# Performance work log

Hardware: AMD Instinct MI355X
Metric: run time of the kernel (lower is better)

## Reference

```python
import jax, jax.numpy as jnp
import numpy as np

# Nemotron-H Mamba2 mixer decoder layer (prefill path, zero initial states,
# full context lengths). Dims per init_kwargs.
B, S, H = 1, 256, 4096
NH, P, G, N, K = 128, 64, 8, 128, 4   # num_heads, head_dim, n_groups, ssm_state_size, conv_kernel
D_INNER = NH * P                      # 8192
D_STATE = G * N                       # 1024
CONV_DIM = D_INNER + 2 * D_STATE      # 10240
IN_OUT = D_INNER + CONV_DIM + NH      # 18560
EPS = 1e-6


def setup_inputs() -> dict:
    key = jax.random.key(0)
    ks = jax.random.split(key, 8)
    sc = 0.02
    return {
        "hidden_states": jax.random.normal(ks[0], (B, S, H), jnp.float32),
        "conv_state": jnp.zeros((B, CONV_DIM, K - 1), jnp.float32),
        "ssm_state": jnp.zeros((B, NH, P, N), jnp.float32),
        "norm_weight": jnp.ones((H,), jnp.float32),
        "w_in": jax.random.normal(ks[1], (IN_OUT, H), jnp.float32) * sc,
        "conv_w": jax.random.normal(ks[2], (CONV_DIM, K), jnp.float32) * 0.2,
        "conv_b": jnp.zeros((CONV_DIM,), jnp.float32),
        "A_log": jax.random.uniform(ks[3], (NH,), jnp.float32, 0.0, 1.0),
        "D_param": jax.random.normal(ks[4], (NH,), jnp.float32) * 0.1,
        "dt_bias": jax.random.normal(ks[5], (NH,), jnp.float32) * 0.1,
        "ssm_norm_weight": jnp.ones((D_INNER,), jnp.float32),
        "w_out": jax.random.normal(ks[6], (H, D_INNER), jnp.float32) * sc,
    }


def _rmsnorm(x, w, eps=EPS):
    var = jnp.mean(x * x, axis=-1, keepdims=True)
    return x * jax.lax.rsqrt(var + eps) * w


def reference(hidden_states, conv_state, ssm_state, norm_weight, w_in, conv_w,
              conv_b, A_log, D_param, dt_bias, ssm_norm_weight, w_out):
    resid = hidden_states
    h = _rmsnorm(hidden_states, norm_weight)           # pre-mixer RMSNorm
    proj = jnp.einsum('bsh,oh->bso', h, w_in)          # in_proj [B,S,18560]
    gate = proj[..., :D_INNER]
    xconv = proj[..., D_INNER:D_INNER + CONV_DIM]
    dt = proj[..., D_INNER + CONV_DIM:]                # [B,S,NH]

    # depthwise causal conv1d, initial left context = conv_state
    xc = jnp.swapaxes(xconv, 1, 2)                     # [B,CONV_DIM,S]
    xpad = jnp.concatenate([conv_state, xc], axis=-1)  # [B,CONV_DIM,S+K-1]
    conv_state_out = xpad[:, :, -(K - 1):]
    y = conv_b[None, :, None]
    for j in range(K):                                 # K=4 taps, unrolled
        y = y + conv_w[:, j][None, :, None] * xpad[:, :, j:j + S]
    y = jax.nn.silu(jnp.swapaxes(y, 1, 2))             # [B,S,CONV_DIM]

    xs = y[..., :D_INNER].reshape(B, S, NH, P)
    Bs = y[..., D_INNER:D_INNER + D_STATE].reshape(B, S, G, N)
    Cs = y[..., D_INNER + D_STATE:].reshape(B, S, G, N)

    A = -jnp.exp(A_log)                                # [NH]
    dtp = jax.nn.softplus(dt + dt_bias)                # [B,S,NH]
    rep = NH // G
    Bh = jnp.repeat(Bs, rep, axis=2)                   # [B,S,NH,N]
    Ch = jnp.repeat(Cs, rep, axis=2)

    def step(state, inp):
        x_t, b_t, c_t, dt_t = inp                      # [B,NH,P],[B,NH,N],[B,NH,N],[B,NH]
        dA = jnp.exp(dt_t * A)                         # [B,NH]
        state = state * dA[..., None, None] + (dt_t[..., None] * x_t)[..., None] * b_t[:, :, None, :]
        y_t = jnp.einsum('bhpn,bhn->bhp', state, c_t)
        return state, y_t

    inps = (jnp.swapaxes(xs, 0, 1), jnp.swapaxes(Bh, 0, 1),
            jnp.swapaxes(Ch, 0, 1), jnp.swapaxes(dtp, 0, 1))
    ssm_state_out, ys = jax.lax.scan(step, ssm_state, inps)
    ys = jnp.swapaxes(ys, 0, 1) + D_param[None, None, :, None] * xs
    ssm_out = ys.reshape(B, S, D_INNER)

    # gated grouped RMSNorm (group_size = D_INNER // G = 1024)
    gated = ssm_out * jax.nn.silu(gate)
    gsize = D_INNER // G
    gg = gated.reshape(B, S, D_INNER // gsize, gsize)
    var = jnp.mean(gg * gg, axis=-1, keepdims=True)
    normed = (gg * jax.lax.rsqrt(var + EPS)).reshape(B, S, D_INNER) * ssm_norm_weight

    out = jnp.einsum('bsd,hd->bsh', normed, w_out)     # out_proj
    return resid + out, conv_state_out, ssm_state_out
```

## Files before the change

### kernel.cpp

```cpp
#include <hip/hip_runtime.h>
#include <hip/hip_bf16.h>

#define Sq 256
#define Hd 4096
#define NH 128
#define Pd 64
#define Gg 8
#define Nn 128
#define D_INNER 8192
#define D_STATE 1024
#define CONV_DIM 10240
#define IN_OUT 18560
#define DT_COL0 18432
#define EPSI 1e-6f

typedef _Float16 f16x8 __attribute__((ext_vector_type(8)));
typedef _Float16 f16x2 __attribute__((ext_vector_type(2)));
typedef float f32x4 __attribute__((ext_vector_type(4)));

__device__ inline ushort f2h(float f) {
  _Float16 h = (_Float16)f;
  return __builtin_bit_cast(ushort, h);
}
__device__ inline float h2f(ushort u) {
  return (float)__builtin_bit_cast(_Float16, u);
}
__device__ inline ushort f2h_lo(float f, ushort hi) {
  float hf = (float)__builtin_bit_cast(_Float16, hi);
  _Float16 l = (_Float16)(f - hf);
  return __builtin_bit_cast(ushort, l);
}
__device__ inline f16x2 pkrtz(float a, float b) {
  return __builtin_bit_cast(f16x2, __builtin_amdgcn_cvt_pkrtz(a, b));
}

__global__ __launch_bounds__(256) void rmsnorm_k(const float* __restrict__ x,
                                                 const float* __restrict__ w,
                                                 ushort* __restrict__ h_hi,
                                                 ushort* __restrict__ h_lo) {
  int s = blockIdx.x, t = threadIdx.x;
  const float4* row = reinterpret_cast<const float4*>(x + (size_t)s * Hd);
  const float4* wv  = reinterpret_cast<const float4*>(w);
  float4 v[4];
  float ss = 0.f;
#pragma unroll
  for (int i = 0; i < 4; i++) {
    v[i] = row[t + i * 256];
    ss += v[i].x * v[i].x + v[i].y * v[i].y + v[i].z * v[i].z + v[i].w * v[i].w;
  }
#pragma unroll
  for (int off = 32; off > 0; off >>= 1) ss += __shfl_xor(ss, off);
  __shared__ float red[4];
  if ((t & 63) == 0) red[t >> 6] = ss;
  __syncthreads();
  ss = red[0] + red[1] + red[2] + red[3];
  float scale = rsqrtf(ss * (1.f / (float)Hd) + EPSI);
  ushort4* hh = reinterpret_cast<ushort4*>(h_hi + (size_t)s * Hd);
  ushort4* hl = reinterpret_cast<ushort4*>(h_lo + (size_t)s * Hd);
#pragma unroll
  for (int i = 0; i < 4; i++) {
    float4 wi = wv[t + i * 256];
    float f0 = v[i].x * scale * wi.x, f1 = v[i].y * scale * wi.y;
    float f2 = v[i].z * scale * wi.z, f3 = v[i].w * scale * wi.w;
    ushort4 oh, ol;
    oh.x = f2h(f0); ol.x = f2h_lo(f0, oh.x);
    oh.y = f2h(f1); ol.y = f2h_lo(f1, oh.y);
    oh.z = f2h(f2); ol.z = f2h_lo(f2, oh.z);
    oh.w = f2h(f3); ol.w = f2h_lo(f3, oh.w);
    hh[t + i * 256] = oh;
    hl[t + i * 256] = ol;
  }
}

__global__ __launch_bounds__(512) void gemm_w256(const ushort* __restrict__ A,
                                                 const float* __restrict__ B,
                                                 float* __restrict__ C0,
                                                 ushort* __restrict__ Cp,
                                                 int ldc, int K, int kLen) {
  __shared__ __align__(16) ushort As[2][256 * 32];
  __shared__ __align__(16) ushort Bs[2][128 * 32];
  int t = threadIdx.x;
  int wave = t >> 6, lane = t & 63;
  int wr = wave >> 1, wc = wave & 1;
  int frow = lane & 15, gq = lane >> 4;
  int bcol = blockIdx.x * 128;
  int z = blockIdx.z;
  int kStart = z * kLen;

  int ar = t >> 2;
  int ax = (ar >> 1) & 3;
  const ushort* ApG0 = A + (size_t)ar * K + kStart + ((t & 3) ^ ax) * 8;
  const ushort* ApG1 = ApG0 + (size_t)128 * K;
  char* dstA0 = (char*)&As[0][0] + wave * 1024;
  char* dstA1 = (char*)&As[0][0] + 8192 + wave * 1024;

  int brow = t >> 2, bq4 = t & 3;
  int bx = (brow >> 1) & 3;
  const float* BpG = B + (size_t)(bcol + brow) * K + kStart + bq4 * 8;
  int bslot = ((bq4) ^ bx) * 16;
  float4 rb[2];

  f32x4 acc[4][4] = {};
  const int NT = kLen / 32;

#define ISSUE_B(kk) { rb[0] = *(const float4*)(BpG + (kk)); \
                      rb[1] = *(const float4*)(BpG + (kk) + 4); }
#define DMA_A(p, kk) { \
    __builtin_amdgcn_global_load_lds( \
        (const __attribute__((address_space(1))) void*)(ApG0 + (kk)), \
        (__attribute__((address_space(3))) void*)(dstA0 + (p) * 16384), 16, 0, 0); \
    __builtin_amdgcn_global_load_lds( \
        (const __attribute__((address_space(1))) void*)(ApG1 + (kk)), \
        (__attribute__((address_space(3))) void*)(dstA1 + (p) * 16384), 16, 0, 0); }
#define WRITE_B(p) { \
    union { f16x2 h2[4]; uint4 q; } u; \
    u.h2[0] = pkrtz(rb[0].x, rb[0].y); u.h2[1] = pkrtz(rb[0].z, rb[0].w); \
    u.h2[2] = pkrtz(rb[1].x, rb[1].y); u.h2[3] = pkrtz(rb[1].z, rb[1].w); \
    *(uint4*)((char*)&Bs[0][0] + (p) * 8192 + brow * 64 + bslot) = u.q; }

  ISSUE_B(0)
  DMA_A(0, 0)
  WRITE_B(0)
  __syncthreads();

  for (int i = 0; i < NT; ++i) {
    int cur = i & 1;
    if (i + 1 < NT) {
      ISSUE_B((i + 1) * 32)
      DMA_A(cur ^ 1, (i + 1) * 32)
    }
    f16x8 af[4], bf[4];
#pragma unroll
    for (int m = 0; m < 4; ++m) {
      int row = wr * 64 + m * 16 + frow;
      af[m] = *(const f16x8*)((const char*)&As[0][0] + cur * 16384 + row * 64 +
                              ((gq ^ ((row >> 1) & 3)) * 16));
    }
#pragma unroll
    for (int n = 0; n < 4; ++n) {
      int row = wc * 64 + n * 16 + frow;
      bf[n] = *(const f16x8*)((const char*)&Bs[0][0] + cur * 8192 + row * 64 +
                              ((gq ^ ((row >> 1) & 3)) * 16));
    }
#pragma unroll
    for (int m = 0; m < 4; ++m)
#pragma unroll
      for (int n = 0; n < 4; ++n)
        acc[m][n] = __builtin_amdgcn_mfma_f32_16x16x32_f16(af[m], bf[n], acc[m][n], 0, 0, 0);
    __builtin_amdgcn_sched_barrier(0);
    if (i + 1 < NT) WRITE_B(cur ^ 1)
    __syncthreads();
  }
#undef ISSUE_B
#undef DMA_A
#undef WRITE_B

  if (z == 0) {
#pragma unroll
    for (int m = 0; m < 4; ++m) {
      int row0 = wr * 64 + m * 16 + (lane >> 4) * 4;
#pragma unroll
      for (int n = 0; n < 4; ++n) {
        int col = bcol + wc * 64 + n * 16 + frow;
#pragma unroll
        for (int r = 0; r < 4; ++r)
          C0[(size_t)(row0 + r) * ldc + col] = acc[m][n][r];
      }
    }
  } else {
    ushort* Cz = Cp + (size_t)(z - 1) * Sq * ldc;
#pragma unroll
    for (int m = 0; m < 4; ++m) {
      int row0 = wr * 64 + m * 16 + (lane >> 4) * 4;
#pragma unroll
      for (int n = 0; n < 4; ++n) {
        int col = bcol + wc * 64 + n * 16 + frow;
#pragma unroll
        for (int r = 0; r < 4; ++r)
          Cz[(size_t)(row0 + r) * ldc + col] = f2h(acc[m][n][r]);
      }
    }
  }
}

template<int BN, bool SPLIT>
__global__ __launch_bounds__(256) void gemm_mfma(const ushort* __restrict__ A_hi,
                                                 const ushort* __restrict__ A_lo,
                                                 const float* __restrict__ B,
                                                 float* __restrict__ C,
                                                 int ldc, int K, int kLen,
                                                 int bcol0, int M) {
  constexpr int BK = 64;
  constexpr int LDA = 72;
  constexpr int N_REP = BN / 32;
  constexpr int BQN = (BN == 128) ? 8 : 4;
  __shared__ __align__(16) ushort As[64 * LDA];
  __shared__ __align__(16) ushort Bs[BN * LDA];
  __shared__ __align__(16) ushort AsL[SPLIT ? 64 * LDA : 1];
  __shared__ __align__(16) ushort BsL[SPLIT ? BN * LDA : 1];

  int t = threadIdx.x;
  int wave = t >> 6, lane = t & 63;
  int wr = wave >> 1, wc = wave & 1;
  int frow = lane & 15, fk = (lane >> 4) * 8;
  int rowBase = blockIdx.x * 64;
  int bcol = bcol0 + blockIdx.y * BN;
  int ccol = blockIdx.y * BN;
  int kStart = blockIdx.z * kLen;
  C += (size_t)blockIdx.z * M * ldc;

  int arow = t >> 2, ak = (t & 3) * 16;
  const ushort* Ap  = A_hi + (size_t)(rowBase + arow) * K + ak;
  const ushort* ApL = SPLIT ? (A_lo + (size_t)(rowBase + arow) * K + ak) : nullptr;

  int brow, bq;
  if constexpr (BN == 128) { brow = t >> 1; bq = (t & 1) * 32; }
  else                     { brow = t >> 2; bq = (t & 3) * 16; }
  const float* Bp = B + (size_t)(bcol + brow) * K + bq;

  f32x4 acc[2][N_REP] = {};
  uint4 aPre[2], aPreL[2];
  float4 bPre[BQN];

  auto loadK = [&](int kk) {
    aPre[0] = *reinterpret_cast<const uint4*>(Ap + kk);
    aPre[1] = *reinterpret_cast<const uint4*>(Ap + kk + 8);
    if constexpr (SPLIT) {
      aPreL[0] = *reinterpret_cast<const uint4*>(ApL + kk);
      aPreL[1] = *reinterpret_cast<const uint4*>(ApL + kk + 8);
    }
#pragma unroll
    for (int j = 0; j < BQN; ++j)
      bPre[j] = *reinterpret_cast<const float4*>(Bp + kk + j * 4);
  };

  loadK(kStart);
  for (int ki = 0; ki < kLen; ki += BK) {
    __syncthreads();
    *reinterpret_cast<uint4*>(&As[arow * LDA + ak])     = aPre[0];
    *reinterpret_cast<uint4*>(&As[arow * LDA + ak + 8]) = aPre[1];
    if constexpr (SPLIT) {
      *reinterpret_cast<uint4*>(&AsL[arow * LDA + ak])     = aPreL[0];
      *reinterpret_cast<uint4*>(&AsL[arow * LDA + ak + 8]) = aPreL[1];
    }
    {
      ushort hb[BQN * 4];
      ushort lb[SPLIT ? BQN * 4 : 1];
      const float* bf = reinterpret_cast<const float*>(bPre);
#pragma unroll
      for (int j = 0; j < BQN * 4; ++j) {
        hb[j] = f2h(bf[j]);
        if constexpr (SPLIT) lb[j] = f2h_lo(bf[j], hb[j]);
      }
#pragma unroll
      for (int j = 0; j < BQN / 2; ++j)
        *reinterpret_cast<uint4*>(&Bs[brow * LDA + bq + j * 8]) =
            reinterpret_cast<const uint4*>(hb)[j];
      if constexpr (SPLIT) {
#pragma unroll
        for (int j = 0; j < BQN / 2; ++j)
          *reinterpret_cast<uint4*>(&BsL[brow * LDA + bq + j * 8]) =
              reinterpret_cast<const uint4*>(lb)[j];
      }
    }
    __syncthreads();
    if (ki + BK < kLen) loadK(kStart + ki + BK);
    f16x8 af[2][2], bfv[N_REP][2];
    f16x8 afL[SPLIT ? 2 : 1][2], bfL[SPLIT ? N_REP : 1][2];
#pragma unroll
    for (int m = 0; m < 2; ++m)
#pragma unroll
      for (int kh = 0; kh < 2; ++kh) {
        af[m][kh] = *reinterpret_cast<const f16x8*>(
            &As[(wr * 32 + m * 16 + frow) * LDA + kh * 32 + fk]);
        if constexpr (SPLIT)
          afL[m][kh] = *reinterpret_cast<const f16x8*>(
              &AsL[(wr * 32 + m * 16 + frow) * LDA + kh * 32 + fk]);
      }
#pragma unroll
    for (int n = 0; n < N_REP; ++n)
#pragma unroll
      for (int kh = 0; kh < 2; ++kh) {
        bfv[n][kh] = *reinterpret_cast<const f16x8*>(
            &Bs[(wc * (BN / 2) + n * 16 + frow) * LDA + kh * 32 + fk]);
        if constexpr (SPLIT)
          bfL[n][kh] = *reinterpret_cast<const f16x8*>(
              &BsL[(wc * (BN / 2) + n * 16 + frow) * LDA + kh * 32 + fk]);
      }
#pragma unroll
    for (int kh = 0; kh < 2; ++kh)
#pragma unroll
      for (int m = 0; m < 2; ++m)
#pragma unroll
        for (int n = 0; n < N_REP; ++n) {
          acc[m][n] = __builtin_amdgcn_mfma_f32_16x16x32_f16(af[m][kh], bfv[n][kh], acc[m][n], 0, 0, 0);
          if constexpr (SPLIT) {
            acc[m][n] = __builtin_amdgcn_mfma_f32_16x16x32_f16(af[m][kh], bfL[n][kh], acc[m][n], 0, 0, 0);
            acc[m][n] = __builtin_amdgcn_mfma_f32_16x16x32_f16(afL[m][kh], bfv[n][kh], acc[m][n], 0, 0, 0);
          }
        }
  }

#pragma unroll
  for (int m = 0; m < 2; ++m) {
    int row0 = rowBase + wr * 32 + m * 16 + (lane >> 4) * 4;
#pragma unroll
    for (int n = 0; n < N_REP; ++n) {
      int col = ccol + wc * (BN / 2) + n * 16 + frow;
#pragma unroll
      for (int r = 0; r < 4; ++r)
        C[(size_t)(row0 + r) * ldc + col] = acc[m][n][r];
    }
  }
}

__global__ __launch_bounds__(256) void reduce_in_k(float* __restrict__ proj,
                                                   const ushort* __restrict__ pp) {
  int i = blockIdx.x * 256 + threadIdx.x;
  const size_t PL = (size_t)Sq * IN_OUT;
  float4 o = reinterpret_cast<const float4*>(proj)[i];
#pragma unroll
  for (int zz = 0; zz < 3; ++zz) {
    ushort4 hv = reinterpret_cast<const ushort4*>(pp + zz * PL)[i];
    o.x += h2f(hv.x); o.y += h2f(hv.y); o.z += h2f(hv.z); o.w += h2f(hv.w);
  }
  reinterpret_cast<float4*>(proj)[i] = o;
}

__global__ __launch_bounds__(256) void conv_silu_k(const float* __restrict__ proj,
                                                   const float* __restrict__ cstate,
                                                   const float* __restrict__ cw,
                                                   const float* __restrict__ cb,
                                                   float* __restrict__ y,
                                                   float* __restrict__ out1) {
  int s = blockIdx.y;
  if (s == Sq) {
    int c = blockIdx.x * 256 + threadIdx.x;
#pragma unroll
    for (int tt = 0; tt < 3; ++tt)
      out1[c * 3 + tt] = proj[(size_t)(Sq - 3 + tt) * IN_OUT + D_INNER + c];
    return;
  }
  int c = blockIdx.x * 256 + threadIdx.x;
  float acc = cb[c];
  float4 w4 = *reinterpret_cast<const float4*>(cw + c * 4);
  float wj[4] = {w4.x, w4.y, w4.z, w4.w};
#pragma unroll
  for (int j = 0; j < 4; j++) {
    int si = s + j - 3;
    float v = (si < 0) ? cstate[c * 3 + (si + 3)]
                       : proj[(size_t)si * IN_OUT + D_INNER + c];
    acc += wj[j] * v;
  }
  float sig = 1.f / (1.f + expf(-acc));
  y[(size_t)s * CONV_DIM + c] = acc * sig;
}

#define CS 16
__global__ __launch_bounds__(256) void ssm_scan_k(const float* __restrict__ y_conv,
                                                  const float* __restrict__ dtfix,
                                                  const float* __restrict__ dt_bias,
                                                  const float* __restrict__ sstate_in,
                                                  const float* __restrict__ A_log,
                                                  const float* __restrict__ D_param,
                                                  float* __restrict__ ys_out,
                                                  float* __restrict__ sstate_out) {
  int h = blockIdx.x >> 2;
  int pb = (blockIdx.x & 3) * 16;
  int t = threadIdx.x;
  int ng = t & 15, pl = t >> 4;
  int g = h >> 4;
  float A = -expf(A_log[h]);
  float Dp = D_param[h];
  float bias = dt_bias[h];

  float st[8];
  {
    const float* sp = sstate_in + ((size_t)h * Pd + pb + pl) * Nn + ng * 8;
    float4 v = *reinterpret_cast<const float4*>(sp);
    float4 w = *reinterpret_cast<const float4*>(sp + 4);
    st[0] = v.x; st[1] = v.y; st[2] = v.z; st[3] = v.w;
    st[4] = w.x; st[5] = w.y; st[6] = w.z; st[7] = w.w;
  }

  __shared__ __align__(16) float ybuf[CS][272];
  __shared__ float dts[CS];
  int lr = t >> 4;
  int lc = t & 15;

  for (int ch = 0; ch < Sq / CS; ++ch) {
    int s0 = ch * CS;
    __syncthreads();
    const float* rowp = y_conv + (size_t)(s0 + lr) * CONV_DIM;
#pragma unroll
    for (int j = 0; j < 5; ++j) {
      int c = lc + 16 * j;
      if (c < 68) {
        const float* src;
        int off;
        if (c < 4)       { src = rowp + h * 64 + pb;                      off = c * 4; }
        else if (c < 36) { src = rowp + D_INNER + g * 128;                off = (c - 4) * 4; }
        else             { src = rowp + D_INNER + D_STATE + g * 128;      off = (c - 36) * 4; }
        int dst = (c < 4) ? c * 4 : (c < 36 ? 16 + (c - 4) * 4 : 144 + (c - 36) * 4);
        *reinterpret_cast<float4*>(&ybuf[lr][dst]) = *reinterpret_cast<const float4*>(src + off);
      }
    }
    if (t < CS) {
      float v = bias;
      int idx = (s0 + t) * NH + h;
#pragma unroll
      for (int zz = 0; zz < 32; ++zz) v += dtfix[zz * (Sq * NH) + idx];
      dts[t] = (v > 20.f) ? v : log1pf(expf(v));
    }
    __syncthreads();

#pragma unroll 4
    for (int stp = 0; stp < CS; ++stp) {
      float dt = dts[stp];
      float dA = expf(dt * A);
      float x0 = ybuf[stp][pl];
      float dtx = dt * x0;
      float4 b0 = *reinterpret_cast<const float4*>(&ybuf[stp][16 + ng * 8]);
      float4 b1 = *reinterpret_cast<const float4*>(&ybuf[stp][16 + ng * 8 + 4]);
      float4 c0 = *reinterpret_cast<const float4*>(&ybuf[stp][144 + ng * 8]);
      float4 c1 = *reinterpret_cast<const float4*>(&ybuf[stp][144 + ng * 8 + 4]);
      float y0;
      st[0] = st[0] * dA + dtx * b0.x;  y0  = st[0] * c0.x;
      st[1] = st[1] * dA + dtx * b0.y;  y0 += st[1] * c0.y;
      st[2] = st[2] * dA + dtx * b0.z;  y0 += st[2] * c0.z;
      st[3] = st[3] * dA + dtx * b0.w;  y0 += st[3] * c0.w;
      st[4] = st[4] * dA + dtx * b1.x;  y0 += st[4] * c1.x;
      st[5] = st[5] * dA + dtx * b1.y;  y0 += st[5] * c1.y;
      st[6] = st[6] * dA + dtx * b1.z;  y0 += st[6] * c1.z;
      st[7] = st[7] * dA + dtx * b1.w;  y0 += st[7] * c1.w;
      y0 += __shfl_xor(y0, 1); y0 += __shfl_xor(y0, 2);
      y0 += __shfl_xor(y0, 4); y0 += __shfl_xor(y0, 8);
      if (ng == 0)
        ys_out[(size_t)(s0 + stp) * D_INNER + h * 64 + pb + pl] = y0 + Dp * x0;
    }
  }

  float* so = sstate_out + ((size_t)h * Pd + pb + pl) * Nn + ng * 8;
  *reinterpret_cast<float4*>(so)     = make_float4(st[0], st[1], st[2], st[3]);
  *reinterpret_cast<float4*>(so + 4) = make_float4(st[4], st[5], st[6], st[7]);
}

__global__ __launch_bounds__(256) void gated_norm_k(const float* __restrict__ ys,
                                                    const float* __restrict__ proj,
                                                    const float* __restrict__ w,
                                                    ushort* __restrict__ out_h) {
  int s = blockIdx.x, g = blockIdx.y, t = threadIdx.x;
  float vals[4];
  float ss = 0.f;
#pragma unroll
  for (int i = 0; i < 4; i++) {
    int d = g * 1024 + i * 256 + t;
    float gate = proj[(size_t)s * IN_OUT + d];
    float v = ys[(size_t)s * D_INNER + d] * (gate / (1.f + expf(-gate)));
    vals[i] = v;
    ss += v * v;
  }
#pragma unroll
  for (int off = 32; off > 0; off >>= 1) ss += __shfl_xor(ss, off);
  __shared__ float red[4];
  if ((t & 63) == 0) red[t >> 6] = ss;
  __syncthreads();
  ss = red[0] + red[1] + red[2] + red[3];
  float scale = rsqrtf(ss * (1.f / 1024.f) + EPSI);
#pragma unroll
  for (int i = 0; i < 4; i++) {
    int d = g * 1024 + i * 256 + t;
    out_h[(size_t)s * D_INNER + d] = f2h(vals[i] * scale * w[d]);
  }
}

__global__ __launch_bounds__(256) void reduce_out_k(const float* __restrict__ p0,
                                                    const ushort* __restrict__ pph,
                                                    const float* __restrict__ hidden,
                                                    float* __restrict__ out0) {
  int i = blockIdx.x * 256 + threadIdx.x;
  const size_t PL = (size_t)Sq * Hd;
  float4 o = reinterpret_cast<const float4*>(hidden)[i];
  float4 a = reinterpret_cast<const float4*>(p0)[i];
  o.x += a.x; o.y += a.y; o.z += a.z; o.w += a.w;
#pragma unroll
  for (int zz = 0; zz < 15; ++zz) {
    ushort4 hv = reinterpret_cast<const ushort4*>(pph + zz * PL)[i];
    o.x += h2f(hv.x); o.y += h2f(hv.y); o.z += h2f(hv.z); o.w += h2f(hv.w);
  }
  reinterpret_cast<float4*>(out0)[i] = o;
}

extern "C" void kernel_launch(void* const* d_in, const int* in_sizes, int n_in,
                              void* d_out, int out_size, void* d_ws, size_t ws_size,
                              hipStream_t stream) {
  const float* hidden    = (const float*)d_in[0];
  const float* cstate_in = (const float*)d_in[1];
  const float* sstate_in = (const float*)d_in[2];
  const float* norm_w    = (const float*)d_in[3];
  const float* w_in      = (const float*)d_in[4];
  const float* conv_w    = (const float*)d_in[5];
  const float* conv_b    = (const float*)d_in[6];
  const float* A_log     = (const float*)d_in[7];
  const float* D_param   = (const float*)d_in[8];
  const float* dt_bias   = (const float*)d_in[9];
  const float* ssm_nw    = (const float*)d_in[10];
  const float* w_out     = (const float*)d_in[11];

  float* out0 = (float*)d_out;
  float* out1 = out0 + (size_t)Sq * Hd;
  float* out2 = out1 + (size_t)CONV_DIM * 3;

  ushort* h_hi  = (ushort*)d_ws;
  ushort* h_lo  = h_hi + (size_t)Sq * Hd;
  float*  proj  = (float*)(h_lo + (size_t)Sq * Hd);
  ushort* pp_in = (ushort*)(proj + (size_t)Sq * IN_OUT);
  float*  y_conv = (float*)pp_in;
  float*  dtp   = y_conv + (size_t)Sq * CONV_DIM;
  float*  ys    = dtp + (size_t)Sq * NH;
  ushort* ys_h  = (ushort*)(ys + (size_t)Sq * D_INNER);
  float*  dtfix = (float*)(ys_h + (size_t)Sq * D_INNER);
  float*  op0    = (float*)d_ws;
  ushort* pp_out = (ushort*)(op0 + (size_t)Sq * Hd);

  rmsnorm_k<<<Sq, 256, 0, stream>>>(hidden, norm_w, h_hi, h_lo);
  gemm_w256<<<dim3(IN_OUT / 128, 1, 4), 512, 0, stream>>>(
      h_hi, w_in, proj, pp_in, IN_OUT, Hd, Hd / 4);
  reduce_in_k<<<(Sq * IN_OUT / 4) / 256, 256, 0, stream>>>(proj, pp_in);
  gemm_mfma<64, true><<<dim3(4, 2, 32), 256, 0, stream>>>(
      h_hi, h_lo, w_in, dtfix, NH, Hd, Hd / 32, DT_COL0, Sq);
  conv_silu_k<<<dim3(CONV_DIM / 256, Sq + 1), 256, 0, stream>>>(
      proj, cstate_in, conv_w, conv_b, y_conv, out1);
  ssm_scan_k<<<NH * 4, 256, 0, stream>>>(y_conv, dtfix, dt_bias, sstate_in,
                                         A_log, D_param, ys, out2);
  gated_norm_k<<<dim3(Sq, Gg), 256, 0, stream>>>(ys, proj, ssm_nw, ys_h);
  gemm_w256<<<dim3(Hd / 128, 1, 16), 512, 0, stream>>>(
      ys_h, w_out, op0, pp_out, Hd, D_INNER, D_INNER / 16);
  reduce_out_k<<<(Sq * Hd / 4) / 256, 256, 0, stream>>>(op0, pp_out, hidden, out0);
}
```

Before: 345.6 us.

## Restructure weight GEMM into 64-wide tiles with BK=64 and split-phase barrier pipeline

```diff
diff --git a/kernel.cpp b/kernel.cpp
--- a/kernel.cpp
+++ b/kernel.cpp
@@ -72,96 +72,123 @@
   }
 }
 
-__global__ __launch_bounds__(512) void gemm_w256(const ushort* __restrict__ A,
-                                                 const float* __restrict__ B,
-                                                 float* __restrict__ C0,
-                                                 ushort* __restrict__ Cp,
-                                                 int ldc, int K, int kLen) {
-  __shared__ __align__(16) ushort As[2][256 * 32];
-  __shared__ __align__(16) ushort Bs[2][128 * 32];
+__global__ __launch_bounds__(512) void gemm_8p(const ushort* __restrict__ A,
+                                               const float* __restrict__ B,
+                                               float* __restrict__ C0,
+                                               ushort* __restrict__ Cp,
+                                               int ldc, int K, int kLen) {
+  __shared__ __align__(16) ushort As[2][256 * 64];
+  __shared__ __align__(16) ushort Bs[2][64 * 64];
   int t = threadIdx.x;
   int wave = t >> 6, lane = t & 63;
   int wr = wave >> 1, wc = wave & 1;
   int frow = lane & 15, gq = lane >> 4;
-  int bcol = blockIdx.x * 128;
+  int bcol = blockIdx.x * 64;
   int z = blockIdx.z;
   int kStart = z * kLen;
 
-  int ar = t >> 2;
-  int ax = (ar >> 1) & 3;
-  const ushort* ApG0 = A + (size_t)ar * K + kStart + ((t & 3) ^ ax) * 8;
-  const ushort* ApG1 = ApG0 + (size_t)128 * K;
-  char* dstA0 = (char*)&As[0][0] + wave * 1024;
-  char* dstA1 = (char*)&As[0][0] + 8192 + wave * 1024;
-
-  int brow = t >> 2, bq4 = t & 3;
-  int bx = (brow >> 1) & 3;
-  const float* BpG = B + (size_t)(bcol + brow) * K + kStart + bq4 * 8;
-  int bslot = ((bq4) ^ bx) * 16;
+  int agl = (lane & 7) ^ (lane >> 3);
+  const ushort* ApG = A + (size_t)(wave * 8 + (lane >> 3)) * K + kStart + agl * 8;
+
+  int brow = t >> 3, bgp = t & 7;
+  int bgl = bgp ^ (brow & 7);
+  const float* BpG = B + (size_t)(bcol + brow) * K + kStart + bgl * 8;
+  int bDst = brow * 128 + bgp * 16;
+
+  f32x4 acc[4][2] = {};
   float4 rb[2];
-
-  f32x4 acc[4][4] = {};
-  const int NT = kLen / 32;
-
-#define ISSUE_B(kk) { rb[0] = *(const float4*)(BpG + (kk)); \
-                      rb[1] = *(const float4*)(BpG + (kk) + 4); }
-#define DMA_A(p, kk) { \
+  const int NT = kLen / 64;
+
+#define SB() __builtin_amdgcn_sched_barrier(0)
+#define ISSUE_RB(kk) { rb[0] = *(const float4*)(BpG + (kk)); \
+                       rb[1] = *(const float4*)(BpG + (kk) + 4); }
+#define DMA_A4(buf, kk) { _Pragma("unroll") for (int p = 0; p < 4; ++p) \
     __builtin_amdgcn_global_load_lds( \
-        (const __attribute__((address_space(1))) void*)(ApG0 + (kk)), \
-        (__attribute__((address_space(3))) void*)(dstA0 + (p) * 16384), 16, 0, 0); \
-    __builtin_amdgcn_global_load_lds( \
-        (const __attribute__((address_space(1))) void*)(ApG1 + (kk)), \
-        (__attribute__((address_space(3))) void*)(dstA1 + (p) * 16384), 16, 0, 0); }
-#define WRITE_B(p) { \
-    union { f16x2 h2[4]; uint4 q; } u; \
+        (const __attribute__((address_space(1))) void*)(ApG + (size_t)p * 64 * K + (kk)), \
+        (__attribute__((address_space(3))) void*)((char*)&As[0][0] + (buf) * 32768 + p * 8192 + wave * 1024), \
+        16, 0, 0); }
+#define WRITE_RB(buf) { union { f16x2 h2[4]; uint4 q; } u; \
     u.h2[0] = pkrtz(rb[0].x, rb[0].y); u.h2[1] = pkrtz(rb[0].z, rb[0].w); \
     u.h2[2] = pkrtz(rb[1].x, rb[1].y); u.h2[3] = pkrtz(rb[1].z, rb[1].w); \
-    *(uint4*)((char*)&Bs[0][0] + (p) * 8192 + brow * 64 + bslot) = u.q; }
-
-  ISSUE_B(0)
-  DMA_A(0, 0)
-  WRITE_B(0)
+    *(uint4*)((char*)&Bs[0][0] + (buf) * 8192 + bDst) = u.q; }
+
+  ISSUE_RB(0)
+  DMA_A4(0, 0)
+  WRITE_RB(0)
   __syncthreads();
 
+  f16x8 af[4][2];
   for (int i = 0; i < NT; ++i) {
-    int cur = i & 1;
-    if (i + 1 < NT) {
-      ISSUE_B((i + 1) * 32)
-      DMA_A(cur ^ 1, (i + 1) * 32)
-    }
-    f16x8 af[4], bf[4];
-#pragma unroll
-    for (int m = 0; m < 4; ++m) {
-      int row = wr * 64 + m * 16 + frow;
-      af[m] = *(const f16x8*)((const char*)&As[0][0] + cur * 16384 + row * 64 +
-                              ((gq ^ ((row >> 1) & 3)) * 16));
-    }
-#pragma unroll
-    for (int n = 0; n < 4; ++n) {
-      int row = wc * 64 + n * 16 + frow;
-      bf[n] = *(const f16x8*)((const char*)&Bs[0][0] + cur * 8192 + row * 64 +
-                              ((gq ^ ((row >> 1) & 3)) * 16));
-    }
+    int cur = i & 1, nxt = cur ^ 1;
+    bool nx = (i + 1 < NT);
+    if (nx) { ISSUE_RB((i + 1) * 64) DMA_A4(nxt, (i + 1) * 64) }
+    SB();
+    if (nx) { asm volatile("s_waitcnt vmcnt(6)" ::: "memory"); }
+    else    { asm volatile("s_waitcnt vmcnt(0)" ::: "memory"); }
+    SB();
+    __builtin_amdgcn_s_barrier();
+    SB();
+    f16x8 bfp[2];
 #pragma unroll
     for (int m = 0; m < 4; ++m)
 #pragma unroll
-      for (int n = 0; n < 4; ++n)
-        acc[m][n] = __builtin_amdgcn_mfma_f32_16x16x32_f16(af[m], bf[n], acc[m][n], 0, 0, 0);
-    __builtin_amdgcn_sched_barrier(0);
-    if (i + 1 < NT) WRITE_B(cur ^ 1)
-    __syncthreads();
-  }
-#undef ISSUE_B
-#undef DMA_A
-#undef WRITE_B
+      for (int kh = 0; kh < 2; ++kh) {
+        int row = wr * 64 + m * 16 + frow;
+        af[m][kh] = *(const f16x8*)((const char*)&As[0][0] + cur * 32768 + row * 128 +
+                                    ((((kh << 2) | gq) ^ (row & 7)) << 4));
+      }
+    {
+      int row = wc * 32 + frow;
+#pragma unroll
+      for (int kh = 0; kh < 2; ++kh)
+        bfp[kh] = *(const f16x8*)((const char*)&Bs[0][0] + cur * 8192 + row * 128 +
+                                  ((((kh << 2) | gq) ^ (row & 7)) << 4));
+    }
+    asm volatile("s_waitcnt lgkmcnt(0)" ::: "memory");
+    SB();
+    __builtin_amdgcn_s_setprio(1);
+#pragma unroll
+    for (int kh = 0; kh < 2; ++kh)
+#pragma unroll
+      for (int m = 0; m < 4; ++m)
+        acc[m][0] = __builtin_amdgcn_mfma_f32_16x16x32_f16(af[m][kh], bfp[kh], acc[m][0], 0, 0, 0);
+    __builtin_amdgcn_s_setprio(0);
+    SB();
+    __builtin_amdgcn_s_barrier();
+    SB();
+    if (nx) WRITE_RB(nxt)
+    {
+      int row = wc * 32 + 16 + frow;
+#pragma unroll
+      for (int kh = 0; kh < 2; ++kh)
+        bfp[kh] = *(const f16x8*)((const char*)&Bs[0][0] + cur * 8192 + row * 128 +
+                                  ((((kh << 2) | gq) ^ (row & 7)) << 4));
+    }
+    asm volatile("s_waitcnt lgkmcnt(0)" ::: "memory");
+    SB();
+    __builtin_amdgcn_s_setprio(1);
+#pragma unroll
+    for (int kh = 0; kh < 2; ++kh)
+#pragma unroll
+      for (int m = 0; m < 4; ++m)
+        acc[m][1] = __builtin_amdgcn_mfma_f32_16x16x32_f16(af[m][kh], bfp[kh], acc[m][1], 0, 0, 0);
+    __builtin_amdgcn_s_setprio(0);
+    SB();
+    __builtin_amdgcn_s_barrier();
+    SB();
+  }
+#undef SB
+#undef ISSUE_RB
+#undef DMA_A4
+#undef WRITE_RB
 
   if (z == 0) {
 #pragma unroll
     for (int m = 0; m < 4; ++m) {
       int row0 = wr * 64 + m * 16 + (lane >> 4) * 4;
 #pragma unroll
-      for (int n = 0; n < 4; ++n) {
-        int col = bcol + wc * 64 + n * 16 + frow;
+      for (int n = 0; n < 2; ++n) {
+        int col = bcol + wc * 32 + n * 16 + frow;
 #pragma unroll
         for (int r = 0; r < 4; ++r)
           C0[(size_t)(row0 + r) * ldc + col] = acc[m][n][r];
@@ -173,8 +200,8 @@
     for (int m = 0; m < 4; ++m) {
       int row0 = wr * 64 + m * 16 + (lane >> 4) * 4;
 #pragma unroll
-      for (int n = 0; n < 4; ++n) {
-        int col = bcol + wc * 64 + n * 16 + frow;
+      for (int n = 0; n < 2; ++n) {
+        int col = bcol + wc * 32 + n * 16 + frow;
 #pragma unroll
         for (int r = 0; r < 4; ++r)
           Cz[(size_t)(row0 + r) * ldc + col] = f2h(acc[m][n][r]);
@@ -524,7 +551,7 @@
   ushort* pp_out = (ushort*)(op0 + (size_t)Sq * Hd);
 
   rmsnorm_k<<<Sq, 256, 0, stream>>>(hidden, norm_w, h_hi, h_lo);
-  gemm_w256<<<dim3(IN_OUT / 128, 1, 4), 512, 0, stream>>>(
+  gemm_8p<<<dim3(IN_OUT / 64, 1, 4), 512, 0, stream>>>(
       h_hi, w_in, proj, pp_in, IN_OUT, Hd, Hd / 4);
   reduce_in_k<<<(Sq * IN_OUT / 4) / 256, 256, 0, stream>>>(proj, pp_in);
   gemm_mfma<64, true><<<dim3(4, 2, 32), 256, 0, stream>>>(
@@ -534,7 +561,7 @@
   ssm_scan_k<<<NH * 4, 256, 0, stream>>>(y_conv, dtfix, dt_bias, sstate_in,
                                          A_log, D_param, ys, out2);
   gated_norm_k<<<dim3(Sq, Gg), 256, 0, stream>>>(ys, proj, ssm_nw, ys_h);
-  gemm_w256<<<dim3(Hd / 128, 1, 16), 512, 0, stream>>>(
+  gemm_8p<<<dim3(Hd / 64, 1, 16), 512, 0, stream>>>(
       ys_h, w_out, op0, pp_out, Hd, D_INNER, D_INNER / 16);
   reduce_out_k<<<(Sq * Hd / 4) / 256, 256, 0, stream>>>(op0, pp_out, hidden, out0);
 }
```

Result: faster. 321.8 us (-6.9%).
